# Kernel tuning notes

Hardware: AMD Instinct MI355X
Metric: run time of the kernel (lower is better)

## Reference

```python
import jax, jax.numpy as jnp
from jax import lax
import numpy as np

B, T, F, N = 64, 12, 64, 1024   # batch, horizon, input feat, n_sensors
H = 256                          # n_hid


def _gru_layer(x, h, Wx, Wh, b):
    # x: (B, Fin, N), h: (B, H, N); weights act on the feature axis, shared across sensors
    gx = jnp.einsum('bfn,fg->bgn', x, Wx) + b[None, :, None]  # (B, 3H, N)
    gh = jnp.einsum('bhn,hg->bgn', h, Wh)                      # (B, 3H, N)
    xr, xz, xn = jnp.split(gx, 3, axis=1)
    hr, hz, hn = jnp.split(gh, 3, axis=1)
    r = jax.nn.sigmoid(xr + hr)
    z = jax.nn.sigmoid(xz + hz)
    n = jnp.tanh(xn + r * hn)
    return (1.0 - z) * n + z * h


def setup_inputs() -> dict:
    key = jax.random.key(0)
    ks = jax.random.split(key, 7)
    x = jax.random.normal(ks[0], (B, T, F, N), dtype=jnp.float32)
    s_in = 1.0 / np.sqrt(F)
    s_h = 1.0 / np.sqrt(H)
    Wx0 = jax.random.normal(ks[1], (F, 3 * H), dtype=jnp.float32) * s_in
    Wh0 = jax.random.normal(ks[2], (H, 3 * H), dtype=jnp.float32) * s_h
    b0 = jnp.zeros((3 * H,), dtype=jnp.float32)
    Wx1 = jax.random.normal(ks[3], (H, 3 * H), dtype=jnp.float32) * s_h
    Wh1 = jax.random.normal(ks[4], (H, 3 * H), dtype=jnp.float32) * s_h
    b1 = jnp.zeros((3 * H,), dtype=jnp.float32)
    return {"x": x, "Wx0": Wx0, "Wh0": Wh0, "b0": b0,
            "Wx1": Wx1, "Wh1": Wh1, "b1": b1}


def reference(x, Wx0, Wh0, b0, Wx1, Wh1, b1):
    b_, t_, f_, n_ = x.shape
    h0 = (jnp.zeros((b_, H, n_), x.dtype), jnp.zeros((b_, H, n_), x.dtype))
    xs = jnp.moveaxis(x, 1, 0)  # (T, B, F, N) scan over horizon

    def step(hs, xt):
        h1 = _gru_layer(xt, hs[0], Wx0, Wh0, b0)
        h2 = _gru_layer(h1, hs[1], Wx1, Wh1, b1)
        return (h1, h2), None

    hs, _ = lax.scan(step, h0, xs)
    # original returns ht: list of final hidden states of all stacked layers
    return jnp.stack(hs)  # (n_layers=2, B, H, N)
```

## Files before the change

kernel.cpp:

```cpp
#include <hip/hip_runtime.h>
#include <hip/hip_fp16.h>
#include <cstdint>
#include <cstddef>

#define Bb 64
#define Tt 12
#define Ff 64
#define Nn 1024
#define Hh 256
#define Gg 768
#define BN 65536

using f32x4 = __attribute__((ext_vector_type(4))) float;
using h8    = __attribute__((ext_vector_type(8))) _Float16;

__device__ __forceinline__ float sigm(float x) {
    return 1.0f / (1.0f + __expf(-x));
}
__device__ __forceinline__ float tanh_fast(float x) {
    return 1.0f - 2.0f / (1.0f + __expf(2.0f * x));
}

__global__ __launch_bounds__(256) void pack_w(
    const float* __restrict__ Wx0, const float* __restrict__ Wh0,
    const float* __restrict__ Wx1, const float* __restrict__ Wh1,
    _Float16* __restrict__ pWx0, _Float16* __restrict__ pWh0,
    _Float16* __restrict__ pWx1, _Float16* __restrict__ pWh1)
{
    int tid = blockIdx.x * 256 + threadIdx.x;
    const int L0 = (Ff / 32) * 48 * 64;
    const int L1 = (Hh / 32) * 48 * 64;
    const float* src; _Float16* dst; int fl;
    if (tid < L0)                { src = Wx0; dst = pWx0; fl = tid; }
    else if (tid < L0 + L1)      { src = Wh0; dst = pWh0; fl = tid - L0; }
    else if (tid < L0 + 2 * L1)  { src = Wx1; dst = pWx1; fl = tid - L0 - L1; }
    else if (tid < L0 + 3 * L1)  { src = Wh1; dst = pWh1; fl = tid - L0 - 2 * L1; }
    else return;
    int lane = fl & 63;
    int rest = fl >> 6;
    int gi   = rest % 48;
    int k32  = rest / 48;
    int krow = k32 * 32 + 8 * (lane >> 4);
    int gcol = gi * 16 + (lane & 15);
    h8 v;
    #pragma unroll
    for (int j = 0; j < 8; ++j) v[j] = (_Float16)src[(size_t)(krow + j) * Gg + gcol];
    *reinterpret_cast<h8*>(dst + (size_t)fl * 8) = v;
}

__global__ __launch_bounds__(256) void tx_kernel(const float* __restrict__ x,
                                                 _Float16* __restrict__ xT)
{
    int nb = blockIdx.x;
    int t  = blockIdx.y;
    int b  = blockIdx.z;
    __shared__ float lds[64][65];
    int tid = threadIdx.x;
    int n0 = nb * 64;
    const float* xp = x + (((size_t)b * Tt + t) * Ff) * Nn + n0;
    #pragma unroll
    for (int it = 0; it < 16; ++it) {
        int idx = it * 256 + tid;
        int f = idx >> 6, n = idx & 63;
        lds[f][n] = xp[(size_t)f * Nn + n];
    }
    __syncthreads();
    int ni = tid >> 2, f0 = (tid & 3) * 16;
    h8 v0, v1;
    #pragma unroll
    for (int j = 0; j < 8; ++j) {
        v0[j] = (_Float16)lds[f0 + j][ni];
        v1[j] = (_Float16)lds[f0 + 8 + j][ni];
    }
    _Float16* dst = xT + ((size_t)t * BN + (size_t)b * Nn + n0 + ni) * Ff + f0;
    reinterpret_cast<h8*>(dst)[0] = v0;
    reinterpret_cast<h8*>(dst)[1] = v1;
}

template<int K1, bool FIRST>
__global__ __launch_bounds__(512, 2) void gru_step(
    const _Float16* __restrict__ A1,
    const _Float16* __restrict__ A2,
    const _Float16* __restrict__ pWx,
    const _Float16* __restrict__ pWh,
    const float* __restrict__ bias,
    _Float16* __restrict__ hout)
{
    int tid  = threadIdx.x;
    int lane = tid & 63;
    int wid  = tid >> 6;
    int rg   = wid >> 2;
    int cg   = wid & 3;
    int m0   = blockIdx.x * 64 + rg * 32;
    int y    = blockIdx.y;
    int l15  = lane & 15, l4 = lane >> 4;
    int gib  = y * 8 + cg * 2;

    const f32x4 z4 = {0.0f, 0.0f, 0.0f, 0.0f};
    f32x4 aR[2][2], aZ[2][2], aN[2][2], aH[2][2];
    #pragma unroll
    for (int i = 0; i < 2; ++i)
        #pragma unroll
        for (int j = 0; j < 2; ++j) { aR[i][j] = z4; aZ[i][j] = z4; aN[i][j] = z4; aH[i][j] = z4; }

    {
        const _Float16* a1p = A1 + (size_t)(m0 + l15) * K1 + 8 * l4;
        #pragma unroll 2
        for (int k0 = 0; k0 < K1; k0 += 32) {
            h8 a0 = *reinterpret_cast<const h8*>(a1p + k0);
            h8 a1 = *reinterpret_cast<const h8*>(a1p + 16 * K1 + k0);
            const _Float16* wp = pWx + ((size_t)(k0 >> 5) * 48) * 512 + (size_t)lane * 8;
            #pragma unroll
            for (int cf = 0; cf < 2; ++cf) {
                h8 bR = *reinterpret_cast<const h8*>(wp + (gib + cf) * 512);
                h8 bZ = *reinterpret_cast<const h8*>(wp + (gib + cf + 16) * 512);
                h8 bN = *reinterpret_cast<const h8*>(wp + (gib + cf + 32) * 512);
                aR[0][cf] = __builtin_amdgcn_mfma_f32_16x16x32_f16(a0, bR, aR[0][cf], 0, 0, 0);
                aR[1][cf] = __builtin_amdgcn_mfma_f32_16x16x32_f16(a1, bR, aR[1][cf], 0, 0, 0);
                aZ[0][cf] = __builtin_amdgcn_mfma_f32_16x16x32_f16(a0, bZ, aZ[0][cf], 0, 0, 0);
                aZ[1][cf] = __builtin_amdgcn_mfma_f32_16x16x32_f16(a1, bZ, aZ[1][cf], 0, 0, 0);
                aN[0][cf] = __builtin_amdgcn_mfma_f32_16x16x32_f16(a0, bN, aN[0][cf], 0, 0, 0);
                aN[1][cf] = __builtin_amdgcn_mfma_f32_16x16x32_f16(a1, bN, aN[1][cf], 0, 0, 0);
            }
        }
    }
    if (!FIRST) {
        const _Float16* a2p = A2 + (size_t)(m0 + l15) * Hh + 8 * l4;
        #pragma unroll 2
        for (int k0 = 0; k0 < Hh; k0 += 32) {
            h8 a0 = *reinterpret_cast<const h8*>(a2p + k0);
            h8 a1 = *reinterpret_cast<const h8*>(a2p + 16 * Hh + k0);
            const _Float16* wp = pWh + ((size_t)(k0 >> 5) * 48) * 512 + (size_t)lane * 8;
            #pragma unroll
            for (int cf = 0; cf < 2; ++cf) {
                h8 bR = *reinterpret_cast<const h8*>(wp + (gib + cf) * 512);
                h8 bZ = *reinterpret_cast<const h8*>(wp + (gib + cf + 16) * 512);
                h8 bN = *reinterpret_cast<const h8*>(wp + (gib + cf + 32) * 512);
                aR[0][cf] = __builtin_amdgcn_mfma_f32_16x16x32_f16(a0, bR, aR[0][cf], 0, 0, 0);
                aR[1][cf] = __builtin_amdgcn_mfma_f32_16x16x32_f16(a1, bR, aR[1][cf], 0, 0, 0);
                aZ[0][cf] = __builtin_amdgcn_mfma_f32_16x16x32_f16(a0, bZ, aZ[0][cf], 0, 0, 0);
                aZ[1][cf] = __builtin_amdgcn_mfma_f32_16x16x32_f16(a1, bZ, aZ[1][cf], 0, 0, 0);
                aH[0][cf] = __builtin_amdgcn_mfma_f32_16x16x32_f16(a0, bN, aH[0][cf], 0, 0, 0);
                aH[1][cf] = __builtin_amdgcn_mfma_f32_16x16x32_f16(a1, bN, aH[1][cf], 0, 0, 0);
            }
        }
    }

    int cb = y * 128 + cg * 32;
    #pragma unroll
    for (int cf = 0; cf < 2; ++cf) {
        int c = cb + cf * 16 + l15;
        float brv = bias[c], bzv = bias[Hh + c], bnv = bias[2 * Hh + c];
        #pragma unroll
        for (int mf = 0; mf < 2; ++mf) {
            int rbase = m0 + mf * 16 + 4 * l4;
            #pragma unroll
            for (int q = 0; q < 4; ++q) {
                size_t idx = (size_t)(rbase + q) * Hh + c;
                float r  = sigm(aR[mf][cf][q] + brv);
                float zt = sigm(aZ[mf][cf][q] + bzv);
                float hn = FIRST ? 0.0f : aH[mf][cf][q];
                float n  = tanh_fast(aN[mf][cf][q] + bnv + r * hn);
                float hp = FIRST ? 0.0f : (float)A2[idx];
                float hv = n + zt * (hp - n);
                hout[idx] = (_Float16)hv;
            }
        }
    }
}

__global__ __launch_bounds__(256) void tout_kernel(const _Float16* __restrict__ hA,
                                                   const _Float16* __restrict__ hB,
                                                   float* __restrict__ out)
{
    int nb = blockIdx.x;
    int cb = blockIdx.y;
    int lb = blockIdx.z;
    int l = lb >> 6, b = lb & 63;
    const _Float16* h = l ? hB : hA;
    __shared__ float lds[64][65];
    int tid = threadIdx.x;
    int n0 = nb * 64, c0 = cb * 64;
    #pragma unroll
    for (int it = 0; it < 16; ++it) {
        int idx = it * 256 + tid;
        int ni = idx >> 6, c = idx & 63;
        lds[ni][c] = (float)h[(size_t)(b * Nn + n0 + ni) * Hh + c0 + c];
    }
    __syncthreads();
    #pragma unroll
    for (int it = 0; it < 16; ++it) {
        int idx = it * 256 + tid;
        int ci = idx >> 6, nj = idx & 63;
        out[(((size_t)l * Bb + b) * Hh + c0 + ci) * Nn + n0 + nj] = lds[nj][ci];
    }
}

extern "C" void kernel_launch(void* const* d_in, const int* in_sizes, int n_in,
                              void* d_out, int out_size, void* d_ws, size_t ws_size,
                              hipStream_t stream)
{
    const float* x   = (const float*)d_in[0];
    const float* Wx0 = (const float*)d_in[1];
    const float* Wh0 = (const float*)d_in[2];
    const float* b0  = (const float*)d_in[3];
    const float* Wx1 = (const float*)d_in[4];
    const float* Wh1 = (const float*)d_in[5];
    const float* b1  = (const float*)d_in[6];
    float* out = (float*)d_out;

    char* ws = (char*)d_ws;
    size_t off = 0;
    auto alloc = [&](size_t bytes) -> void* {
        void* p = ws + off;
        off += (bytes + 255) & ~(size_t)255;
        return p;
    };
    _Float16* xT   = (_Float16*)alloc((size_t)Tt * BN * Ff * 2);
    _Float16* hA0  = (_Float16*)alloc((size_t)BN * Hh * 2);
    _Float16* hA1  = (_Float16*)alloc((size_t)BN * Hh * 2);
    _Float16* hB0  = (_Float16*)alloc((size_t)BN * Hh * 2);
    _Float16* hB1  = (_Float16*)alloc((size_t)BN * Hh * 2);
    _Float16* pWx0 = (_Float16*)alloc((size_t)(Ff / 32) * 48 * 512 * 2);
    _Float16* pWh0 = (_Float16*)alloc((size_t)(Hh / 32) * 48 * 512 * 2);
    _Float16* pWx1 = (_Float16*)alloc((size_t)(Hh / 32) * 48 * 512 * 2);
    _Float16* pWh1 = (_Float16*)alloc((size_t)(Hh / 32) * 48 * 512 * 2);

    pack_w<<<312, 256, 0, stream>>>(Wx0, Wh0, Wx1, Wh1, pWx0, pWh0, pWx1, pWh1);
    tx_kernel<<<dim3(16, Tt, Bb), 256, 0, stream>>>(x, xT);

    _Float16* hA[2] = {hA0, hA1};
    _Float16* hB[2] = {hB0, hB1};
    for (int t = 0; t < Tt; ++t) {
        const _Float16* xt = xT + (size_t)t * BN * Ff;
        _Float16* hAw = hA[t & 1];
        const _Float16* hAr = hA[(t + 1) & 1];
        _Float16* hBw = hB[t & 1];
        const _Float16* hBr = hB[(t + 1) & 1];
        dim3 g(BN / 64, 2);
        if (t == 0) {
            gru_step<Ff, true ><<<g, 512, 0, stream>>>(xt,  hAr, pWx0, pWh0, b0, hAw);
            gru_step<Hh, true ><<<g, 512, 0, stream>>>(hAw, hBr, pWx1, pWh1, b1, hBw);
        } else {
            gru_step<Ff, false><<<g, 512, 0, stream>>>(xt,  hAr, pWx0, pWh0, b0, hAw);
            gru_step<Hh, false><<<g, 512, 0, stream>>>(hAw, hBr, pWx1, pWh1, b1, hBw);
        }
    }
    tout_kernel<<<dim3(16, 4, 2 * Bb), 256, 0, stream>>>(hA[(Tt - 1) & 1], hB[(Tt - 1) & 1], out);
}
```

Baseline: 2.480 ms.

## Stage per-block weight slice in LDS and loop persistent row tiles

```diff
diff --git a/kernel.cpp b/kernel.cpp
--- a/kernel.cpp
+++ b/kernel.cpp
@@ -77,7 +77,7 @@
     reinterpret_cast<h8*>(dst)[1] = v1;
 }
 
-template<int K1, bool FIRST>
+template<int NKX, bool FIRST>
 __global__ __launch_bounds__(512, 2) void gru_step(
     const _Float16* __restrict__ A1,
     const _Float16* __restrict__ A2,
@@ -86,84 +86,105 @@
     const float* __restrict__ bias,
     _Float16* __restrict__ hout)
 {
+    extern __shared__ _Float16 Bs[];
+    constexpr int KX  = NKX * 32;
+    constexpr int NKH = FIRST ? 0 : 8;
+    constexpr int TOTSLOTS = (NKX + NKH) * 6;
+
     int tid  = threadIdx.x;
     int lane = tid & 63;
     int wid  = tid >> 6;
-    int rg   = wid >> 2;
-    int cg   = wid & 3;
-    int m0   = blockIdx.x * 64 + rg * 32;
-    int y    = blockIdx.y;
-    int l15  = lane & 15, l4 = lane >> 4;
-    int gib  = y * 8 + cg * 2;
-
+    int set  = blockIdx.x & 7;
+    int rwg  = blockIdx.x >> 3;
+
+    for (int i = tid; i < TOTSLOTS * 64; i += 512) {
+        int s  = i >> 6;
+        int cl = i & 63;
+        int isWh = (s >= NKX * 6) ? 1 : 0;
+        int sl = isWh ? s - NKX * 6 : s;
+        int k32 = sl / 6, j = sl % 6;
+        int gi  = set * 2 + (j & 1) + (j >> 1) * 16;
+        const _Float16* src = (isWh ? pWh : pWx)
+                            + (size_t)(k32 * 48 + gi) * 512 + cl * 8;
+        *reinterpret_cast<h8*>(&Bs[(size_t)i * 8]) =
+            *reinterpret_cast<const h8*>(src);
+    }
+    __syncthreads();
+
+    int l15 = lane & 15, l4 = lane >> 4;
+    int cb = set * 32;
     const f32x4 z4 = {0.0f, 0.0f, 0.0f, 0.0f};
-    f32x4 aR[2][2], aZ[2][2], aN[2][2], aH[2][2];
-    #pragma unroll
-    for (int i = 0; i < 2; ++i)
+
+    for (int it = 0; it < 4; ++it) {
+        int m0 = rwg * 2048 + it * 512 + wid * 64;
+
+        f32x4 aR[4][2], aZ[4][2], aN[4][2], aH[4][2];
         #pragma unroll
-        for (int j = 0; j < 2; ++j) { aR[i][j] = z4; aZ[i][j] = z4; aN[i][j] = z4; aH[i][j] = z4; }
-
-    {
-        const _Float16* a1p = A1 + (size_t)(m0 + l15) * K1 + 8 * l4;
-        #pragma unroll 2
-        for (int k0 = 0; k0 < K1; k0 += 32) {
-            h8 a0 = *reinterpret_cast<const h8*>(a1p + k0);
-            h8 a1 = *reinterpret_cast<const h8*>(a1p + 16 * K1 + k0);
-            const _Float16* wp = pWx + ((size_t)(k0 >> 5) * 48) * 512 + (size_t)lane * 8;
+        for (int rf = 0; rf < 4; ++rf)
             #pragma unroll
             for (int cf = 0; cf < 2; ++cf) {
-                h8 bR = *reinterpret_cast<const h8*>(wp + (gib + cf) * 512);
-                h8 bZ = *reinterpret_cast<const h8*>(wp + (gib + cf + 16) * 512);
-                h8 bN = *reinterpret_cast<const h8*>(wp + (gib + cf + 32) * 512);
-                aR[0][cf] = __builtin_amdgcn_mfma_f32_16x16x32_f16(a0, bR, aR[0][cf], 0, 0, 0);
-                aR[1][cf] = __builtin_amdgcn_mfma_f32_16x16x32_f16(a1, bR, aR[1][cf], 0, 0, 0);
-                aZ[0][cf] = __builtin_amdgcn_mfma_f32_16x16x32_f16(a0, bZ, aZ[0][cf], 0, 0, 0);
-                aZ[1][cf] = __builtin_amdgcn_mfma_f32_16x16x32_f16(a1, bZ, aZ[1][cf], 0, 0, 0);
-                aN[0][cf] = __builtin_amdgcn_mfma_f32_16x16x32_f16(a0, bN, aN[0][cf], 0, 0, 0);
-                aN[1][cf] = __builtin_amdgcn_mfma_f32_16x16x32_f16(a1, bN, aN[1][cf], 0, 0, 0);
-            }
-        }
-    }
-    if (!FIRST) {
-        const _Float16* a2p = A2 + (size_t)(m0 + l15) * Hh + 8 * l4;
-        #pragma unroll 2
-        for (int k0 = 0; k0 < Hh; k0 += 32) {
-            h8 a0 = *reinterpret_cast<const h8*>(a2p + k0);
-            h8 a1 = *reinterpret_cast<const h8*>(a2p + 16 * Hh + k0);
-            const _Float16* wp = pWh + ((size_t)(k0 >> 5) * 48) * 512 + (size_t)lane * 8;
-            #pragma unroll
-            for (int cf = 0; cf < 2; ++cf) {
-                h8 bR = *reinterpret_cast<const h8*>(wp + (gib + cf) * 512);
-                h8 bZ = *reinterpret_cast<const h8*>(wp + (gib + cf + 16) * 512);
-                h8 bN = *reinterpret_cast<const h8*>(wp + (gib + cf + 32) * 512);
-                aR[0][cf] = __builtin_amdgcn_mfma_f32_16x16x32_f16(a0, bR, aR[0][cf], 0, 0, 0);
-                aR[1][cf] = __builtin_amdgcn_mfma_f32_16x16x32_f16(a1, bR, aR[1][cf], 0, 0, 0);
-                aZ[0][cf] = __builtin_amdgcn_mfma_f32_16x16x32_f16(a0, bZ, aZ[0][cf], 0, 0, 0);
-                aZ[1][cf] = __builtin_amdgcn_mfma_f32_16x16x32_f16(a1, bZ, aZ[1][cf], 0, 0, 0);
-                aH[0][cf] = __builtin_amdgcn_mfma_f32_16x16x32_f16(a0, bN, aH[0][cf], 0, 0, 0);
-                aH[1][cf] = __builtin_amdgcn_mfma_f32_16x16x32_f16(a1, bN, aH[1][cf], 0, 0, 0);
-            }
-        }
-    }
-
-    int cb = y * 128 + cg * 32;
-    #pragma unroll
-    for (int cf = 0; cf < 2; ++cf) {
-        int c = cb + cf * 16 + l15;
-        float brv = bias[c], bzv = bias[Hh + c], bnv = bias[2 * Hh + c];
+                aR[rf][cf] = z4; aZ[rf][cf] = z4; aN[rf][cf] = z4; aH[rf][cf] = z4;
+            }
+
+        {
+            const _Float16* a1p = A1 + (size_t)(m0 + l15) * KX + 8 * l4;
+            #pragma unroll
+            for (int k = 0; k < NKX; ++k) {
+                h8 b[6];
+                #pragma unroll
+                for (int j = 0; j < 6; ++j)
+                    b[j] = *reinterpret_cast<const h8*>(&Bs[(size_t)(k * 6 + j) * 512 + lane * 8]);
+                #pragma unroll
+                for (int rf = 0; rf < 4; ++rf) {
+                    h8 a = *reinterpret_cast<const h8*>(a1p + (size_t)rf * 16 * KX + k * 32);
+                    aR[rf][0] = __builtin_amdgcn_mfma_f32_16x16x32_f16(a, b[0], aR[rf][0], 0, 0, 0);
+                    aR[rf][1] = __builtin_amdgcn_mfma_f32_16x16x32_f16(a, b[1], aR[rf][1], 0, 0, 0);
+                    aZ[rf][0] = __builtin_amdgcn_mfma_f32_16x16x32_f16(a, b[2], aZ[rf][0], 0, 0, 0);
+                    aZ[rf][1] = __builtin_amdgcn_mfma_f32_16x16x32_f16(a, b[3], aZ[rf][1], 0, 0, 0);
+                    aN[rf][0] = __builtin_amdgcn_mfma_f32_16x16x32_f16(a, b[4], aN[rf][0], 0, 0, 0);
+                    aN[rf][1] = __builtin_amdgcn_mfma_f32_16x16x32_f16(a, b[5], aN[rf][1], 0, 0, 0);
+                }
+            }
+        }
+        if (!FIRST) {
+            const _Float16* a2p = A2 + (size_t)(m0 + l15) * Hh + 8 * l4;
+            #pragma unroll
+            for (int k = 0; k < 8; ++k) {
+                h8 b[6];
+                #pragma unroll
+                for (int j = 0; j < 6; ++j)
+                    b[j] = *reinterpret_cast<const h8*>(&Bs[(size_t)((NKX + k) * 6 + j) * 512 + lane * 8]);
+                #pragma unroll
+                for (int rf = 0; rf < 4; ++rf) {
+                    h8 a = *reinterpret_cast<const h8*>(a2p + (size_t)rf * 16 * Hh + k * 32);
+                    aR[rf][0] = __builtin_amdgcn_mfma_f32_16x16x32_f16(a, b[0], aR[rf][0], 0, 0, 0);
+                    aR[rf][1] = __builtin_amdgcn_mfma_f32_16x16x32_f16(a, b[1], aR[rf][1], 0, 0, 0);
+                    aZ[rf][0] = __builtin_amdgcn_mfma_f32_16x16x32_f16(a, b[2], aZ[rf][0], 0, 0, 0);
+                    aZ[rf][1] = __builtin_amdgcn_mfma_f32_16x16x32_f16(a, b[3], aZ[rf][1], 0, 0, 0);
+                    aH[rf][0] = __builtin_amdgcn_mfma_f32_16x16x32_f16(a, b[4], aH[rf][0], 0, 0, 0);
+                    aH[rf][1] = __builtin_amdgcn_mfma_f32_16x16x32_f16(a, b[5], aH[rf][1], 0, 0, 0);
+                }
+            }
+        }
+
         #pragma unroll
-        for (int mf = 0; mf < 2; ++mf) {
-            int rbase = m0 + mf * 16 + 4 * l4;
-            #pragma unroll
-            for (int q = 0; q < 4; ++q) {
-                size_t idx = (size_t)(rbase + q) * Hh + c;
-                float r  = sigm(aR[mf][cf][q] + brv);
-                float zt = sigm(aZ[mf][cf][q] + bzv);
-                float hn = FIRST ? 0.0f : aH[mf][cf][q];
-                float n  = tanh_fast(aN[mf][cf][q] + bnv + r * hn);
-                float hp = FIRST ? 0.0f : (float)A2[idx];
-                float hv = n + zt * (hp - n);
-                hout[idx] = (_Float16)hv;
+        for (int cf = 0; cf < 2; ++cf) {
+            int c = cb + cf * 16 + l15;
+            float brv = bias[c], bzv = bias[Hh + c], bnv = bias[2 * Hh + c];
+            #pragma unroll
+            for (int rf = 0; rf < 4; ++rf) {
+                int rbase = m0 + rf * 16 + 4 * l4;
+                #pragma unroll
+                for (int q = 0; q < 4; ++q) {
+                    size_t idx = (size_t)(rbase + q) * Hh + c;
+                    float r  = sigm(aR[rf][cf][q] + brv);
+                    float zt = sigm(aZ[rf][cf][q] + bzv);
+                    float hn = FIRST ? 0.0f : aH[rf][cf][q];
+                    float n  = tanh_fast(aN[rf][cf][q] + bnv + r * hn);
+                    float hp = FIRST ? 0.0f : (float)A2[idx];
+                    float hv = n + zt * (hp - n);
+                    hout[idx] = (_Float16)hv;
+                }
             }
         }
     }
@@ -226,6 +247,10 @@
     _Float16* pWx1 = (_Float16*)alloc((size_t)(Hh / 32) * 48 * 512 * 2);
     _Float16* pWh1 = (_Float16*)alloc((size_t)(Hh / 32) * 48 * 512 * 2);
 
+    (void)hipFuncSetAttribute(
+        reinterpret_cast<const void*>(&gru_step<8, false>),
+        hipFuncAttributeMaxDynamicSharedMemorySize, 96 * 1024);
+
     pack_w<<<312, 256, 0, stream>>>(Wx0, Wh0, Wx1, Wh1, pWx0, pWh0, pWx1, pWh1);
     tx_kernel<<<dim3(16, Tt, Bb), 256, 0, stream>>>(x, xT);
 
@@ -237,13 +262,12 @@
         const _Float16* hAr = hA[(t + 1) & 1];
         _Float16* hBw = hB[t & 1];
         const _Float16* hBr = hB[(t + 1) & 1];
-        dim3 g(BN / 64, 2);
         if (t == 0) {
-            gru_step<Ff, true ><<<g, 512, 0, stream>>>(xt,  hAr, pWx0, pWh0, b0, hAw);
-            gru_step<Hh, true ><<<g, 512, 0, stream>>>(hAw, hBr, pWx1, pWh1, b1, hBw);
+            gru_step<2, true ><<<256, 512, 12 * 1024, stream>>>(xt,  hAr, pWx0, pWh0, b0, hAw);
+            gru_step<8, true ><<<256, 512, 48 * 1024, stream>>>(hAw, hBr, pWx1, pWh1, b1, hBw);
         } else {
-            gru_step<Ff, false><<<g, 512, 0, stream>>>(xt,  hAr, pWx0, pWh0, b0, hAw);
-            gru_step<Hh, false><<<g, 512, 0, stream>>>(hAw, hBr, pWx1, pWh1, b1, hBw);
+            gru_step<2, false><<<256, 512, 60 * 1024, stream>>>(xt,  hAr, pWx0, pWh0, b0, hAw);
+            gru_step<8, false><<<256, 512, 96 * 1024, stream>>>(hAw, hBr, pWx1, pWh1, b1, hBw);
         }
     }
     tout_kernel<<<dim3(16, 4, 2 * Bb), 256, 0, stream>>>(hA[(Tt - 1) & 1], hB[(Tt - 1) & 1], out);
```

After: 6.085 ms. +145.4%, slower.
